# Optimization experiments

Hardware: AMD Instinct MI355X
Metric: run time of the kernel (lower is better)

The kernel has to match this reference:

```python
import jax, jax.numpy as jnp
import numpy as np

H = 1024; W = 1024
SPACE_SIGMA = 16.0; RANGE_SIGMA = 0.25
PAD_XY = 2; PAD_Z = 2
DIM = 5


def setup_inputs() -> dict:
    key = jax.random.key(0)
    k1, k2 = jax.random.split(key)
    features = jax.random.uniform(k1, (H, W, 3), dtype=jnp.float32)
    inp = jax.random.normal(k2, (H, W, 3), dtype=jnp.float32)
    return {"features": features, "inp": inp}


def _grid_dims(features_np):
    # Grid sizes are data-dependent in the original (TF builds them from
    # per-channel min/max); compute them host-side from concrete inputs.
    sh = int(float(H - 1) / SPACE_SIGMA) + 1 + 2 * PAD_XY
    sw = int(float(W - 1) / SPACE_SIGMA) + 1 + 2 * PAD_XY
    depths = []
    for c in range(3):
        ch = features_np[..., c]
        delta = float(ch.max() - ch.min())
        depths.append(int(delta / RANGE_SIGMA) + 1 + 2 * PAD_Z)
    return (sh, sw, depths[0], depths[1], depths[2])


def _both_indices(size, coord):
    left = jnp.clip(coord.astype(jnp.int32), 0, size - 1)
    right = jnp.clip(left + 1, 0, size - 1)
    return left, right


def _convn(data, n_iter=2):
    # Faithful port of the TF convn: separable [1,2,1]/4 pass per axis with
    # the exact same ping-pong buffer / boundary-keep / transpose behavior.
    buffer = jnp.zeros_like(data)
    perm = (1, 2, 3, 4, 0)
    for _ in range(n_iter):
        buffer, data = data, buffer
        for _ in range(DIM):
            newdata = (buffer[:-2] + buffer[2:] + 2.0 * buffer[1:-1]) / 4.0
            data = jnp.concatenate([data[:1], newdata, data[-1:]], axis=0)
            data = jnp.transpose(data, perm)
            buffer = jnp.transpose(buffer, perm)
    return data


def _filter(features, inp, dims):
    sh, sw, dr, dg, db = dims
    hw = H * W
    yy, xx = jnp.meshgrid(jnp.arange(H, dtype=jnp.float32),
                          jnp.arange(W, dtype=jnp.float32), indexing="ij")
    splat_yy = (yy / SPACE_SIGMA + 0.5).astype(jnp.int32) + PAD_XY
    splat_xx = (xx / SPACE_SIGMA + 0.5).astype(jnp.int32) + PAD_XY
    slice_yy = yy / SPACE_SIGMA + PAD_XY
    slice_xx = xx / SPACE_SIGMA + PAD_XY
    y_i, y_i2 = _both_indices(sh, slice_yy)
    x_i, x_i2 = _both_indices(sw, slice_xx)
    y_alpha = (slice_yy - y_i.astype(jnp.float32)).reshape(-1)
    x_alpha = (slice_xx - x_i.astype(jnp.float32)).reshape(-1)

    chans = []
    for c, depth in zip(range(3), (dr, dg, db)):
        v = features[..., c]
        v0 = v - jnp.min(v)
        splat_v = (v0 / RANGE_SIGMA + 0.5).astype(jnp.int32) + PAD_Z
        slice_v = v0 / RANGE_SIGMA + PAD_Z
        li, ri = _both_indices(depth, slice_v)
        alpha = (slice_v - li.astype(jnp.float32)).reshape(-1)
        chans.append((splat_v, li, ri, alpha))
    (splat_rr, r_i, r_i2, r_alpha) = chans[0]
    (splat_gg, g_i, g_i2, g_alpha) = chans[1]
    (splat_bb, b_i, b_i2, b_alpha) = chans[2]

    splat_coords = ((((splat_yy * sw + splat_xx) * dr + splat_rr) * dg
                     + splat_gg) * db + splat_bb).reshape(-1)  # [hw]

    idx_all = jnp.stack([y_i, y_i2, x_i, x_i2, r_i, r_i2,
                         g_i, g_i2, b_i, b_i2]).reshape(10, hw)
    alphas_all = jnp.stack([1.0 - y_alpha, y_alpha, 1.0 - x_alpha, x_alpha,
                            1.0 - r_alpha, r_alpha, 1.0 - g_alpha, g_alpha,
                            1.0 - b_alpha, b_alpha])  # [10, hw]

    # 32 corners of the 5-D hypercube; sel[c, d] picks left/right index per dim.
    corners = np.stack(np.meshgrid(*([np.arange(2)] * DIM), indexing="ij"),
                       axis=-1).reshape(-1, DIM)
    sel = corners + np.arange(DIM) * 2  # [32, 5]

    strides = (sw, dr, dg, db)
    coord = idx_all[sel[:, 0]]  # [32, hw]
    for d in range(1, DIM):
        coord = coord * strides[d - 1] + idx_all[sel[:, d]]
    alpha_prod = alphas_all[sel[:, 0]]  # [32, hw]
    for d in range(1, DIM):
        alpha_prod = alpha_prod * alphas_all[sel[:, d]]

    total = sh * sw * dr * dg * db

    def ch_filter(ch):
        grid = jnp.zeros((total,), jnp.float32).at[splat_coords].add(ch.reshape(-1))
        grid = _convn(grid.reshape(sh, sw, dr, dg, db))
        vals = grid.reshape(-1)[coord]  # [32, hw] multilinear gather
        return jnp.sum(alpha_prod * vals, axis=0).reshape(H, W)

    outT = jax.vmap(ch_filter)(jnp.transpose(inp, (2, 0, 1)))
    return jnp.transpose(outT, (1, 2, 0))


def reference(features, inp):
    dims = _grid_dims(np.asarray(features))
    return _filter(features, inp, dims)
```

## Files before the change

kernel.cpp:

```cpp
#include <hip/hip_runtime.h>

namespace {

constexpr int kH  = 1024;
constexpr int kW  = 1024;
constexpr int kHW = kH * kW;
constexpr int kSH = 68;
constexpr int kSW = 68;
constexpr int kD  = 8;
constexpr int kT3 = kSH * kSW * kD * kD * kD;


__global__ void minmax_kernel(const float* __restrict__ feat, float* __restrict__ part) {
    float mn[3] = {1e30f, 1e30f, 1e30f};
    float mx[3] = {-1e30f, -1e30f, -1e30f};
    int tid = blockIdx.x * blockDim.x + threadIdx.x;
    int stride = gridDim.x * blockDim.x;
    for (int p = tid; p < kHW; p += stride) {
        #pragma unroll
        for (int c = 0; c < 3; ++c) {
            float v = feat[p * 3 + c];
            mn[c] = fminf(mn[c], v);
            mx[c] = fmaxf(mx[c], v);
        }
    }
    #pragma unroll
    for (int off = 32; off > 0; off >>= 1) {
        #pragma unroll
        for (int c = 0; c < 3; ++c) {
            mn[c] = fminf(mn[c], __shfl_down(mn[c], off, 64));
            mx[c] = fmaxf(mx[c], __shfl_down(mx[c], off, 64));
        }
    }
    __shared__ float smn[4][3], smx[4][3];
    int wave = threadIdx.x >> 6;
    if ((threadIdx.x & 63) == 0) {
        #pragma unroll
        for (int c = 0; c < 3; ++c) { smn[wave][c] = mn[c]; smx[wave][c] = mx[c]; }
    }
    __syncthreads();
    if (threadIdx.x == 0) {
        #pragma unroll
        for (int c = 0; c < 3; ++c) {
            part[blockIdx.x * 6 + c]     = fminf(fminf(smn[0][c], smn[1][c]), fminf(smn[2][c], smn[3][c]));
            part[blockIdx.x * 6 + 3 + c] = fmaxf(fmaxf(smx[0][c], smx[1][c]), fmaxf(smx[2][c], smx[3][c]));
        }
    }
}

__global__ void params_kernel(const float* __restrict__ part, float* __restrict__ hdrF) {
    int t = threadIdx.x;
    float mn[3], mx[3];
    #pragma unroll
    for (int c = 0; c < 3; ++c) { mn[c] = part[t * 6 + c]; mx[c] = part[t * 6 + 3 + c]; }
    #pragma unroll
    for (int off = 32; off > 0; off >>= 1) {
        #pragma unroll
        for (int c = 0; c < 3; ++c) {
            mn[c] = fminf(mn[c], __shfl_down(mn[c], off, 64));
            mx[c] = fmaxf(mx[c], __shfl_down(mx[c], off, 64));
        }
    }
    __shared__ float smn[4][3], smx[4][3];
    int wave = t >> 6;
    if ((t & 63) == 0) {
        #pragma unroll
        for (int c = 0; c < 3; ++c) { smn[wave][c] = mn[c]; smx[wave][c] = mx[c]; }
    }
    __syncthreads();
    if (t == 0) {
        int* ip = (int*)(hdrF + 8);
        #pragma unroll
        for (int c = 0; c < 3; ++c) {
            float bmn = fminf(fminf(smn[0][c], smn[1][c]), fminf(smn[2][c], smn[3][c]));
            float bmx = fmaxf(fmaxf(smx[0][c], smx[1][c]), fmaxf(smx[2][c], smx[3][c]));
            float delta = bmx - bmn;
            int depth = (int)((double)delta / 0.25) + 1 + 4;
            if (depth > kD) depth = kD;
            if (depth < 1) depth = 1;
            hdrF[c] = bmn;
            ip[c] = depth;
        }
    }
}

__global__ void splat_kernel(const float* __restrict__ feat,
                             const float* __restrict__ inp,
                             const float* __restrict__ hdrF,
                             float* __restrict__ grid) {
    int ix = blockIdx.x, iy = blockIdx.y;
    int y0 = (iy == 0) ? 0 : 16 * iy - 8;
    int x0 = (ix == 0) ? 0 : 16 * ix - 8;
    int h = (iy == 0 || iy == 64) ? 8 : 16;
    int w = (ix == 0 || ix == 64) ? 8 : 16;

    __shared__ float acc[3 * 512];
    for (int i = threadIdx.x; i < 3 * 512; i += 256) acc[i] = 0.0f;
    __syncthreads();

    int t = threadIdx.x;
    int n = w * h;
    if (t < n) {
        int lx = t & (w - 1);
        int ly = (w == 16) ? (t >> 4) : (t >> 3);
        int y = y0 + ly, x = x0 + lx;
        int p = (y << 10) + x;
        float v0 = feat[p * 3 + 0] - hdrF[0];
        float v1 = feat[p * 3 + 1] - hdrF[1];
        float v2 = feat[p * 3 + 2] - hdrF[2];
        int sr = (int)(v0 * 4.0f + 0.5f) + 2;
        int sg = (int)(v1 * 4.0f + 0.5f) + 2;
        int sb = (int)(v2 * 4.0f + 0.5f) + 2;
        int ci = (sr << 6) + (sg << 3) + sb;
        atomicAdd(&acc[ci],            inp[p * 3 + 0]);
        atomicAdd(&acc[512 + ci],      inp[p * 3 + 1]);
        atomicAdd(&acc[1024 + ci],     inp[p * 3 + 2]);
    }
    __syncthreads();

    long base = ((long)((iy + 2) * kSW + (ix + 2))) << 9;
    for (int i = threadIdx.x; i < 512; i += 256) {
        grid[base + i]            = acc[i];
        grid[kT3 + base + i]      = acc[512 + i];
        grid[2 * kT3 + base + i]  = acc[1024 + i];
    }
}

__global__ __launch_bounds__(192) void blur2_kernel(float* __restrict__ dst,
                                                    const float* __restrict__ src,
                                                    const float* __restrict__ hdrF) {
    int cx = blockIdx.x + 2, cy = blockIdx.y + 2;
    const int* ip = (const int*)(hdrF + 8);
    int dr = ip[0], dg = ip[1], db = ip[2];

    __shared__ float Sv[3 * 512];
    long cbase = ((long)(cy * kSW + cx)) << 9;

    {
        const float4* g4 = (const float4*)src;
        for (int i = threadIdx.x; i < 384; i += 192) {
            int ch = i >> 7, i4 = i & 127;
            float4 q = g4[(long)ch * (kT3 / 4) + (cbase >> 2) + i4];
            int rg = i4 >> 1;
            int b0 = (i4 & 1) * 4;
            Sv[ch * 512 + (b0 + 0) * 64 + rg] = q.x;
            Sv[ch * 512 + (b0 + 1) * 64 + rg] = q.y;
            Sv[ch * 512 + (b0 + 2) * 64 + rg] = q.z;
            Sv[ch * 512 + (b0 + 3) * 64 + rg] = q.w;
        }
    }
    __syncthreads();

    int ch = threadIdx.x >> 6;
    int rg = threadIdx.x & 63;
    int r = rg >> 3, g = rg & 7;

    auto SV = [&](int b, int l) -> float { return Sv[ch * 512 + b * 64 + l]; };
    auto gsp = [&](int ccy, int ccx, int rr, int gg, int bb) -> float {
        if (ccy < 2 || ccy > 66 || ccx < 2 || ccx > 66) return 0.0f;
        return src[(long)ch * kT3 + (((long)(ccy * kSW + ccx)) << 9) + (rr << 6) + (gg << 3) + bb];
    };

    bool gI = (g >= 1) && (g <= dg - 2);
    bool rI = (r >= 1) && (r <= dr - 2);

    float v[8];
    #pragma unroll
    for (int b = 0; b < 8; ++b) v[b] = SV(b, rg);

    int eHi = db - 1;

    auto o1_end = [&](int e) -> float {
        float Vm, Vp;
        if (gI)      { Vm = SV(e, rg - 1); Vp = SV(e, rg + 1); }
        else if (rI) { Vm = SV(e, rg - 8); Vp = SV(e, rg + 8); }
        else         { Vm = gsp(cy, cx - 1, r, g, e); Vp = gsp(cy, cx + 1, r, g, e); }
        return (Vm + Vp + 2.0f * SV(e, rg)) * 0.25f;
    };
    float o1_lo = o1_end(0);
    float o1_hi = o1_end(eHi);

    float o1[8];
    #pragma unroll
    for (int b = 0; b < 8; ++b) {
        float iv = 0.0f;
        if (b >= 1 && b <= 6) iv = ((v[b - 1] + v[b + 1]) + 2.0f * v[b]) * 0.25f;
        o1[b] = (b >= 1 && b <= db - 2) ? iv : (b == 0 ? o1_lo : (b == eHi ? o1_hi : 0.0f));
    }

    auto out1_in = [&](int r2, int g2, int e) -> float {
        int l2 = (r2 << 3) + g2;
        float C = SV(e, l2);
        float Nm, Np;
        if (g2 >= 1 && g2 <= dg - 2)      { Nm = SV(e, l2 - 1); Np = SV(e, l2 + 1); }
        else if (r2 >= 1 && r2 <= dr - 2) { Nm = SV(e, l2 - 8); Np = SV(e, l2 + 8); }
        else { Nm = gsp(cy, cx - 1, r2, g2, e); Np = gsp(cy, cx + 1, r2, g2, e); }
        return (Nm + Np + 2.0f * C) * 0.25f;
    };
    auto out1_x = [&](int cx2, int e) -> float {
        float C = gsp(cy, cx2, r, g, e);
        float Nm, Np;
        if (cx2 >= 1 && cx2 <= kSW - 2) { Nm = gsp(cy, cx2 - 1, r, g, e); Np = gsp(cy, cx2 + 1, r, g, e); }
        else                            { Nm = gsp(cy - 1, cx2, r, g, e); Np = gsp(cy + 1, cx2, r, g, e); }
        return (Nm + Np + 2.0f * C) * 0.25f;
    };

    auto o2_end = [&](int e, float o1e) -> float {
        float Xm, Xp;
        if (gI)      { Xm = out1_in(r, g - 1, e); Xp = out1_in(r, g + 1, e); }
        else if (rI) { Xm = out1_in(r - 1, g, e); Xp = out1_in(r + 1, g, e); }
        else         { Xm = out1_x(cx - 1, e);    Xp = out1_x(cx + 1, e); }
        return (Xm + Xp + 2.0f * o1e) * 0.25f;
    };
    float o2_lo = o2_end(0, o1_lo);
    float o2_hi = o2_end(eHi, o1_hi);

    float o2[8];
    #pragma unroll
    for (int b = 0; b < 8; ++b) {
        float iv = 0.0f;
        if (b >= 1 && b <= 6) iv = ((o1[b - 1] + o1[b + 1]) + 2.0f * o1[b]) * 0.25f;
        o2[b] = (b >= 1 && b <= db - 2) ? iv : (b == 0 ? o2_lo : (b == eHi ? o2_hi : 0.0f));
    }

    __syncthreads();
    #pragma unroll
    for (int b = 0; b < 8; ++b) Sv[ch * 512 + b * 64 + rg] = o2[b];
    __syncthreads();

    {
        float4* d4 = (float4*)dst;
        for (int i = threadIdx.x; i < 384; i += 192) {
            int c2 = i >> 7, i4 = i & 127;
            int l2 = i4 >> 1;
            int b0 = (i4 & 1) * 4;
            float4 q = make_float4(Sv[c2 * 512 + (b0 + 0) * 64 + l2],
                                   Sv[c2 * 512 + (b0 + 1) * 64 + l2],
                                   Sv[c2 * 512 + (b0 + 2) * 64 + l2],
                                   Sv[c2 * 512 + (b0 + 3) * 64 + l2]);
            d4[(long)c2 * (kT3 / 4) + (cbase >> 2) + i4] = q;
        }
    }
}

__global__ __launch_bounds__(256) void slice_kernel(const float* __restrict__ feat,
                                                    const float* __restrict__ hdrF,
                                                    const float* __restrict__ grid,
                                                    float* __restrict__ out) {
    __shared__ float sg[3 * 4 * 512];
    int tx = blockIdx.x, ty = blockIdx.y;

    {
        const float4* g4 = (const float4*)grid;
        float4* s4 = (float4*)sg;
        #pragma unroll
        for (int it = 0; it < 2; ++it) {
            int i = threadIdx.x + it * 256;
            int cell = i >> 7;
            int ci4 = i & 127;
            int cy = ty + 2 + (cell >> 1), cx = tx + 2 + (cell & 1);
            long cbase4 = ((long)(cy * kSW + cx)) << 7;
            #pragma unroll
            for (int ch = 0; ch < 3; ++ch)
                s4[ch * 512 + i] = g4[(long)ch * (kT3 / 4) + cbase4 + ci4];
        }
    }
    __syncthreads();

    const int* ip = (const int*)(hdrF + 8);
    int d3[3] = {ip[0], ip[1], ip[2]};
    int lx = threadIdx.x & 15, ly = threadIdx.x >> 4;
    int y = (ty << 4) + ly, x = (tx << 4) + lx;
    int p = (y << 10) + x;

    float ya = (float)ly * 0.0625f;
    float xa = (float)lx * 0.0625f;

    int li[3], ri[3];
    float al[3];
    #pragma unroll
    for (int c = 0; c < 3; ++c) {
        float v0 = feat[p * 3 + c] - hdrF[c];
        float sv = v0 * 4.0f + 2.0f;
        int l = (int)sv;
        int dm = d3[c] - 1;
        l = l < 0 ? 0 : (l > dm ? dm : l);
        int rr = l + 1 > dm ? dm : l + 1;
        li[c] = l; ri[c] = rr; al[c] = sv - (float)l;
    }

    float spw[4];
    {
        float wy[2] = {1.0f - ya, ya};
        float wx[2] = {1.0f - xa, xa};
        spw[0] = wy[0] * wx[0]; spw[1] = wy[0] * wx[1];
        spw[2] = wy[1] * wx[0]; spw[3] = wy[1] * wx[1];
    }
    int cpi[8]; float cpw[8];
    {
        int rs[2] = {li[0], ri[0]}; float wrr[2] = {1.0f - al[0], al[0]};
        int gs[2] = {li[1], ri[1]}; float wgg[2] = {1.0f - al[1], al[1]};
        int bs[2] = {li[2], ri[2]}; float wbb[2] = {1.0f - al[2], al[2]};
        #pragma unroll
        for (int cr = 0; cr < 2; ++cr)
        #pragma unroll
        for (int cg = 0; cg < 2; ++cg)
        #pragma unroll
        for (int cb = 0; cb < 2; ++cb) {
            int k = (cr * 2 + cg) * 2 + cb;
            cpi[k] = (rs[cr] << 6) + (gs[cg] << 3) + bs[cb];
            cpw[k] = (wrr[cr] * wgg[cg]) * wbb[cb];
        }
    }

    float acc0 = 0.0f, acc1 = 0.0f, acc2 = 0.0f;
    #pragma unroll
    for (int k = 0; k < 4; ++k) {
        #pragma unroll
        for (int j = 0; j < 8; ++j) {
            int si = (k << 9) + cpi[j];
            float w = spw[k] * cpw[j];
            acc0 += w * sg[si];
            acc1 += w * sg[2048 + si];
            acc2 += w * sg[4096 + si];
        }
    }
    out[p * 3 + 0] = acc0;
    out[p * 3 + 1] = acc1;
    out[p * 3 + 2] = acc2;
}

}

extern "C" void kernel_launch(void* const* d_in, const int* in_sizes, int n_in,
                              void* d_out, int out_size, void* d_ws, size_t ws_size,
                              hipStream_t stream) {
    const float* feat = (const float*)d_in[0];
    const float* inp  = (const float*)d_in[1];
    float* out = (float*)d_out;

    float* hdrF  = (float*)d_ws;
    float* part  = (float*)((char*)d_ws + 1024);
    float* gridA = (float*)((char*)d_ws + 8192);
    float* gridB = gridA + 3 * (size_t)kT3;

    minmax_kernel<<<256, 256, 0, stream>>>(feat, part);
    params_kernel<<<1, 256, 0, stream>>>(part, hdrF);

    splat_kernel<<<dim3(65, 65), 256, 0, stream>>>(feat, inp, hdrF, gridA);
    blur2_kernel<<<dim3(65, 65), 192, 0, stream>>>(gridB, gridA, hdrF);
    slice_kernel<<<dim3(64, 64), 256, 0, stream>>>(feat, hdrF, gridB, out);
}
```

Measured before the change: 144.0 us.

## Fuse blur into slice kernel, recomputing blurred cells per tile

Merges the blur and slice kernels: each slice block loads its four neighbouring grid cells, blurs them in shared memory, and slices directly from the blurred values in a transposed layout. This removes one kernel launch and the write and re-read of the intermediate blurred grid, while the blurred values are kept in a b-major layout. In exchange, each cell is blurred up to four times by neighbouring blocks, shared memory use rises to 48KB per block, which limits occupancy, and the per-thread loop runs three blur tasks.

```diff
diff --git a/kernel.cpp b/kernel.cpp
--- a/kernel.cpp
+++ b/kernel.cpp
@@ -126,149 +126,117 @@
     }
 }
 
-__global__ __launch_bounds__(192) void blur2_kernel(float* __restrict__ dst,
-                                                    const float* __restrict__ src,
-                                                    const float* __restrict__ hdrF) {
-    int cx = blockIdx.x + 2, cy = blockIdx.y + 2;
+__global__ __launch_bounds__(256) void blur_slice_kernel(const float* __restrict__ feat,
+                                                         const float* __restrict__ hdrF,
+                                                         const float* __restrict__ src,
+                                                         float* __restrict__ out) {
+    __shared__ float Sv[4 * 1536];
+    __shared__ float Sb[4 * 1536];
+    int tx = blockIdx.x, ty = blockIdx.y;
+
     const int* ip = (const int*)(hdrF + 8);
     int dr = ip[0], dg = ip[1], db = ip[2];
-
-    __shared__ float Sv[3 * 512];
-    long cbase = ((long)(cy * kSW + cx)) << 9;
+    int eHi = db - 1;
 
     {
         const float4* g4 = (const float4*)src;
-        for (int i = threadIdx.x; i < 384; i += 192) {
-            int ch = i >> 7, i4 = i & 127;
-            float4 q = g4[(long)ch * (kT3 / 4) + (cbase >> 2) + i4];
+        for (int i = threadIdx.x; i < 1536; i += 256) {
+            int cell = i / 384;
+            int rem = i - cell * 384;
+            int ch = rem >> 7, i4 = rem & 127;
+            int cy = ty + 2 + (cell >> 1), cx = tx + 2 + (cell & 1);
+            long cb4 = ((long)(cy * kSW + cx)) << 7;
+            float4 q = g4[(long)ch * (kT3 / 4) + cb4 + i4];
             int rg = i4 >> 1;
             int b0 = (i4 & 1) * 4;
-            Sv[ch * 512 + (b0 + 0) * 64 + rg] = q.x;
-            Sv[ch * 512 + (b0 + 1) * 64 + rg] = q.y;
-            Sv[ch * 512 + (b0 + 2) * 64 + rg] = q.z;
-            Sv[ch * 512 + (b0 + 3) * 64 + rg] = q.w;
-        }
-    }
-    __syncthreads();
-
-    int ch = threadIdx.x >> 6;
-    int rg = threadIdx.x & 63;
-    int r = rg >> 3, g = rg & 7;
-
-    auto SV = [&](int b, int l) -> float { return Sv[ch * 512 + b * 64 + l]; };
-    auto gsp = [&](int ccy, int ccx, int rr, int gg, int bb) -> float {
-        if (ccy < 2 || ccy > 66 || ccx < 2 || ccx > 66) return 0.0f;
-        return src[(long)ch * kT3 + (((long)(ccy * kSW + ccx)) << 9) + (rr << 6) + (gg << 3) + bb];
-    };
-
-    bool gI = (g >= 1) && (g <= dg - 2);
-    bool rI = (r >= 1) && (r <= dr - 2);
-
-    float v[8];
-    #pragma unroll
-    for (int b = 0; b < 8; ++b) v[b] = SV(b, rg);
-
-    int eHi = db - 1;
-
-    auto o1_end = [&](int e) -> float {
-        float Vm, Vp;
-        if (gI)      { Vm = SV(e, rg - 1); Vp = SV(e, rg + 1); }
-        else if (rI) { Vm = SV(e, rg - 8); Vp = SV(e, rg + 8); }
-        else         { Vm = gsp(cy, cx - 1, r, g, e); Vp = gsp(cy, cx + 1, r, g, e); }
-        return (Vm + Vp + 2.0f * SV(e, rg)) * 0.25f;
-    };
-    float o1_lo = o1_end(0);
-    float o1_hi = o1_end(eHi);
-
-    float o1[8];
-    #pragma unroll
-    for (int b = 0; b < 8; ++b) {
-        float iv = 0.0f;
-        if (b >= 1 && b <= 6) iv = ((v[b - 1] + v[b + 1]) + 2.0f * v[b]) * 0.25f;
-        o1[b] = (b >= 1 && b <= db - 2) ? iv : (b == 0 ? o1_lo : (b == eHi ? o1_hi : 0.0f));
-    }
-
-    auto out1_in = [&](int r2, int g2, int e) -> float {
-        int l2 = (r2 << 3) + g2;
-        float C = SV(e, l2);
-        float Nm, Np;
-        if (g2 >= 1 && g2 <= dg - 2)      { Nm = SV(e, l2 - 1); Np = SV(e, l2 + 1); }
-        else if (r2 >= 1 && r2 <= dr - 2) { Nm = SV(e, l2 - 8); Np = SV(e, l2 + 8); }
-        else { Nm = gsp(cy, cx - 1, r2, g2, e); Np = gsp(cy, cx + 1, r2, g2, e); }
-        return (Nm + Np + 2.0f * C) * 0.25f;
-    };
-    auto out1_x = [&](int cx2, int e) -> float {
-        float C = gsp(cy, cx2, r, g, e);
-        float Nm, Np;
-        if (cx2 >= 1 && cx2 <= kSW - 2) { Nm = gsp(cy, cx2 - 1, r, g, e); Np = gsp(cy, cx2 + 1, r, g, e); }
-        else                            { Nm = gsp(cy - 1, cx2, r, g, e); Np = gsp(cy + 1, cx2, r, g, e); }
-        return (Nm + Np + 2.0f * C) * 0.25f;
-    };
-
-    auto o2_end = [&](int e, float o1e) -> float {
-        float Xm, Xp;
-        if (gI)      { Xm = out1_in(r, g - 1, e); Xp = out1_in(r, g + 1, e); }
-        else if (rI) { Xm = out1_in(r - 1, g, e); Xp = out1_in(r + 1, g, e); }
-        else         { Xm = out1_x(cx - 1, e);    Xp = out1_x(cx + 1, e); }
-        return (Xm + Xp + 2.0f * o1e) * 0.25f;
-    };
-    float o2_lo = o2_end(0, o1_lo);
-    float o2_hi = o2_end(eHi, o1_hi);
-
-    float o2[8];
-    #pragma unroll
-    for (int b = 0; b < 8; ++b) {
-        float iv = 0.0f;
-        if (b >= 1 && b <= 6) iv = ((o1[b - 1] + o1[b + 1]) + 2.0f * o1[b]) * 0.25f;
-        o2[b] = (b >= 1 && b <= db - 2) ? iv : (b == 0 ? o2_lo : (b == eHi ? o2_hi : 0.0f));
-    }
-
-    __syncthreads();
-    #pragma unroll
-    for (int b = 0; b < 8; ++b) Sv[ch * 512 + b * 64 + rg] = o2[b];
-    __syncthreads();
-
-    {
-        float4* d4 = (float4*)dst;
-        for (int i = threadIdx.x; i < 384; i += 192) {
-            int c2 = i >> 7, i4 = i & 127;
-            int l2 = i4 >> 1;
-            int b0 = (i4 & 1) * 4;
-            float4 q = make_float4(Sv[c2 * 512 + (b0 + 0) * 64 + l2],
-                                   Sv[c2 * 512 + (b0 + 1) * 64 + l2],
-                                   Sv[c2 * 512 + (b0 + 2) * 64 + l2],
-                                   Sv[c2 * 512 + (b0 + 3) * 64 + l2]);
-            d4[(long)c2 * (kT3 / 4) + (cbase >> 2) + i4] = q;
-        }
-    }
-}
-
-__global__ __launch_bounds__(256) void slice_kernel(const float* __restrict__ feat,
-                                                    const float* __restrict__ hdrF,
-                                                    const float* __restrict__ grid,
-                                                    float* __restrict__ out) {
-    __shared__ float sg[3 * 4 * 512];
-    int tx = blockIdx.x, ty = blockIdx.y;
-
-    {
-        const float4* g4 = (const float4*)grid;
-        float4* s4 = (float4*)sg;
-        #pragma unroll
-        for (int it = 0; it < 2; ++it) {
-            int i = threadIdx.x + it * 256;
-            int cell = i >> 7;
-            int ci4 = i & 127;
-            int cy = ty + 2 + (cell >> 1), cx = tx + 2 + (cell & 1);
-            long cbase4 = ((long)(cy * kSW + cx)) << 7;
-            #pragma unroll
-            for (int ch = 0; ch < 3; ++ch)
-                s4[ch * 512 + i] = g4[(long)ch * (kT3 / 4) + cbase4 + ci4];
-        }
-    }
-    __syncthreads();
-
-    const int* ip = (const int*)(hdrF + 8);
-    int d3[3] = {ip[0], ip[1], ip[2]};
+            float* S = Sv + cell * 1536 + ch * 512;
+            S[(b0 + 0) * 64 + rg] = q.x;
+            S[(b0 + 1) * 64 + rg] = q.y;
+            S[(b0 + 2) * 64 + rg] = q.z;
+            S[(b0 + 3) * 64 + rg] = q.w;
+        }
+    }
+    __syncthreads();
+
+    #pragma unroll
+    for (int k = 0; k < 3; ++k) {
+        int task = threadIdx.x + (k << 8);
+        int cell = task / 192;
+        int t2 = task - cell * 192;
+        int ch = t2 >> 6;
+        int rg = t2 & 63;
+        int r = rg >> 3, g = rg & 7;
+        int cy = ty + 2 + (cell >> 1), cx = tx + 2 + (cell & 1);
+
+        float* S = Sv + cell * 1536 + ch * 512;
+        auto SV = [&](int b, int l) -> float { return S[b * 64 + l]; };
+        auto gsp = [&](int ccy, int ccx, int rr, int gg, int bb) -> float {
+            if (ccy < 2 || ccy > 66 || ccx < 2 || ccx > 66) return 0.0f;
+            return src[(long)ch * kT3 + (((long)(ccy * kSW + ccx)) << 9) + (rr << 6) + (gg << 3) + bb];
+        };
+
+        bool gI = (g >= 1) && (g <= dg - 2);
+        bool rI = (r >= 1) && (r <= dr - 2);
+
+        float v[8];
+        #pragma unroll
+        for (int b = 0; b < 8; ++b) v[b] = SV(b, rg);
+
+        auto o1_end = [&](int e) -> float {
+            float Vm, Vp;
+            if (gI)      { Vm = SV(e, rg - 1); Vp = SV(e, rg + 1); }
+            else if (rI) { Vm = SV(e, rg - 8); Vp = SV(e, rg + 8); }
+            else         { Vm = gsp(cy, cx - 1, r, g, e); Vp = gsp(cy, cx + 1, r, g, e); }
+            return (Vm + Vp + 2.0f * SV(e, rg)) * 0.25f;
+        };
+        float o1_lo = o1_end(0);
+        float o1_hi = o1_end(eHi);
+
+        float o1[8];
+        #pragma unroll
+        for (int b = 0; b < 8; ++b) {
+            float iv = 0.0f;
+            if (b >= 1 && b <= 6) iv = ((v[b - 1] + v[b + 1]) + 2.0f * v[b]) * 0.25f;
+            o1[b] = (b >= 1 && b <= db - 2) ? iv : (b == 0 ? o1_lo : (b == eHi ? o1_hi : 0.0f));
+        }
+
+        auto out1_in = [&](int r2, int g2, int e) -> float {
+            int l2 = (r2 << 3) + g2;
+            float C = SV(e, l2);
+            float Nm, Np;
+            if (g2 >= 1 && g2 <= dg - 2)      { Nm = SV(e, l2 - 1); Np = SV(e, l2 + 1); }
+            else if (r2 >= 1 && r2 <= dr - 2) { Nm = SV(e, l2 - 8); Np = SV(e, l2 + 8); }
+            else { Nm = gsp(cy, cx - 1, r2, g2, e); Np = gsp(cy, cx + 1, r2, g2, e); }
+            return (Nm + Np + 2.0f * C) * 0.25f;
+        };
+        auto out1_x = [&](int cx2, int e) -> float {
+            float C = gsp(cy, cx2, r, g, e);
+            float Nm, Np;
+            if (cx2 >= 1 && cx2 <= kSW - 2) { Nm = gsp(cy, cx2 - 1, r, g, e); Np = gsp(cy, cx2 + 1, r, g, e); }
+            else                            { Nm = gsp(cy - 1, cx2, r, g, e); Np = gsp(cy + 1, cx2, r, g, e); }
+            return (Nm + Np + 2.0f * C) * 0.25f;
+        };
+        auto o2_end = [&](int e, float o1e) -> float {
+            float Xm, Xp;
+            if (gI)      { Xm = out1_in(r, g - 1, e); Xp = out1_in(r, g + 1, e); }
+            else if (rI) { Xm = out1_in(r - 1, g, e); Xp = out1_in(r + 1, g, e); }
+            else         { Xm = out1_x(cx - 1, e);    Xp = out1_x(cx + 1, e); }
+            return (Xm + Xp + 2.0f * o1e) * 0.25f;
+        };
+        float o2_lo = o2_end(0, o1_lo);
+        float o2_hi = o2_end(eHi, o1_hi);
+
+        float* B = Sb + cell * 1536 + ch * 512;
+        #pragma unroll
+        for (int b = 0; b < 8; ++b) {
+            float iv = 0.0f;
+            if (b >= 1 && b <= 6) iv = ((o1[b - 1] + o1[b + 1]) + 2.0f * o1[b]) * 0.25f;
+            float o2 = (b >= 1 && b <= db - 2) ? iv : (b == 0 ? o2_lo : (b == eHi ? o2_hi : 0.0f));
+            B[b * 64 + rg] = o2;
+        }
+    }
+    __syncthreads();
+
     int lx = threadIdx.x & 15, ly = threadIdx.x >> 4;
     int y = (ty << 4) + ly, x = (tx << 4) + lx;
     int p = (y << 10) + x;
@@ -278,6 +246,7 @@
 
     int li[3], ri[3];
     float al[3];
+    int d3[3] = {dr, dg, db};
     #pragma unroll
     for (int c = 0; c < 3; ++c) {
         float v0 = feat[p * 3 + c] - hdrF[c];
@@ -308,7 +277,7 @@
         #pragma unroll
         for (int cb = 0; cb < 2; ++cb) {
             int k = (cr * 2 + cg) * 2 + cb;
-            cpi[k] = (rs[cr] << 6) + (gs[cg] << 3) + bs[cb];
+            cpi[k] = (bs[cb] << 6) + (rs[cr] << 3) + gs[cg];
             cpw[k] = (wrr[cr] * wgg[cg]) * wbb[cb];
         }
     }
@@ -316,13 +285,14 @@
     float acc0 = 0.0f, acc1 = 0.0f, acc2 = 0.0f;
     #pragma unroll
     for (int k = 0; k < 4; ++k) {
+        const float* B = Sb + k * 1536;
         #pragma unroll
         for (int j = 0; j < 8; ++j) {
-            int si = (k << 9) + cpi[j];
+            int si = cpi[j];
             float w = spw[k] * cpw[j];
-            acc0 += w * sg[si];
-            acc1 += w * sg[2048 + si];
-            acc2 += w * sg[4096 + si];
+            acc0 += w * B[si];
+            acc1 += w * B[512 + si];
+            acc2 += w * B[1024 + si];
         }
     }
     out[p * 3 + 0] = acc0;
@@ -342,12 +312,10 @@
     float* hdrF  = (float*)d_ws;
     float* part  = (float*)((char*)d_ws + 1024);
     float* gridA = (float*)((char*)d_ws + 8192);
-    float* gridB = gridA + 3 * (size_t)kT3;
 
     minmax_kernel<<<256, 256, 0, stream>>>(feat, part);
     params_kernel<<<1, 256, 0, stream>>>(part, hdrF);
 
     splat_kernel<<<dim3(65, 65), 256, 0, stream>>>(feat, inp, hdrF, gridA);
-    blur2_kernel<<<dim3(65, 65), 192, 0, stream>>>(gridB, gridA, hdrF);
-    slice_kernel<<<dim3(64, 64), 256, 0, stream>>>(feat, hdrF, gridB, out);
-}
+    blur_slice_kernel<<<dim3(64, 64), 256, 0, stream>>>(feat, hdrF, gridA, out);
+}
```

Result: slower. 211.9 us (+47.1%).

## Interleave blurred grid channels as float4 and vectorize splat/minmax loads

Applied to the files above, without the earlier changes.

The blur kernel now writes its output as a compact per-cell float4 array with the three channels interleaved. The slice kernel can then fetch all channels of two adjacent b-corners with two float4 LDS reads and lerp along b, replacing 8 scalar corner gathers per channel. The splat kernel stages features and inputs through shared memory with coalesced float4 loads, and minmax reads float4 vectors. The blur shared buffer is padded to stride 72 to cut bank conflicts, at the cost of extra workspace layout assumptions and a 4th padding lane in the float4 grid.

```diff
diff --git a/kernel.cpp b/kernel.cpp
--- a/kernel.cpp
+++ b/kernel.cpp
@@ -9,20 +9,22 @@
 constexpr int kSW = 68;
 constexpr int kD  = 8;
 constexpr int kT3 = kSH * kSW * kD * kD * kD;
-
+constexpr int kNC = 65;
 
 __global__ void minmax_kernel(const float* __restrict__ feat, float* __restrict__ part) {
+    const float4* f4 = (const float4*)feat;
     float mn[3] = {1e30f, 1e30f, 1e30f};
     float mx[3] = {-1e30f, -1e30f, -1e30f};
     int tid = blockIdx.x * blockDim.x + threadIdx.x;
     int stride = gridDim.x * blockDim.x;
-    for (int p = tid; p < kHW; p += stride) {
-        #pragma unroll
-        for (int c = 0; c < 3; ++c) {
-            float v = feat[p * 3 + c];
-            mn[c] = fminf(mn[c], v);
-            mx[c] = fmaxf(mx[c], v);
-        }
+    for (int c = tid; c < kHW / 4; c += stride) {
+        float4 q0 = f4[c * 3], q1 = f4[c * 3 + 1], q2 = f4[c * 3 + 2];
+        mn[0] = fminf(mn[0], fminf(fminf(q0.x, q0.w), fminf(q1.z, q2.y)));
+        mx[0] = fmaxf(mx[0], fmaxf(fmaxf(q0.x, q0.w), fmaxf(q1.z, q2.y)));
+        mn[1] = fminf(mn[1], fminf(fminf(q0.y, q1.x), fminf(q1.w, q2.z)));
+        mx[1] = fmaxf(mx[1], fmaxf(fmaxf(q0.y, q1.x), fmaxf(q1.w, q2.z)));
+        mn[2] = fminf(mn[2], fminf(fminf(q0.z, q1.y), fminf(q2.x, q2.w)));
+        mx[2] = fmaxf(mx[2], fmaxf(fmaxf(q0.z, q1.y), fmaxf(q2.x, q2.w)));
     }
     #pragma unroll
     for (int off = 32; off > 0; off >>= 1) {
@@ -84,10 +86,10 @@
     }
 }
 
-__global__ void splat_kernel(const float* __restrict__ feat,
-                             const float* __restrict__ inp,
-                             const float* __restrict__ hdrF,
-                             float* __restrict__ grid) {
+__global__ __launch_bounds__(256) void splat_kernel(const float* __restrict__ feat,
+                                                    const float* __restrict__ inp,
+                                                    const float* __restrict__ hdrF,
+                                                    float* __restrict__ grid) {
     int ix = blockIdx.x, iy = blockIdx.y;
     int y0 = (iy == 0) ? 0 : 16 * iy - 8;
     int x0 = (ix == 0) ? 0 : 16 * ix - 8;
@@ -95,7 +97,18 @@
     int w = (ix == 0 || ix == 64) ? 8 : 16;
 
     __shared__ float acc[3 * 512];
+    __shared__ float fS[16 * 48], iS[16 * 48];
     for (int i = threadIdx.x; i < 3 * 512; i += 256) acc[i] = 0.0f;
+
+    int rowVec = (w * 3) >> 2;
+    int nvec = h * rowVec;
+    const float4* f4 = (const float4*)(feat + ((long)y0 * kW + x0) * 3);
+    const float4* i4 = (const float4*)(inp  + ((long)y0 * kW + x0) * 3);
+    for (int t = threadIdx.x; t < nvec; t += 256) {
+        int row = t / rowVec, q = t - row * rowVec;
+        ((float4*)fS)[row * rowVec + q] = f4[row * (kW * 3 / 4) + q];
+        ((float4*)iS)[row * rowVec + q] = i4[row * (kW * 3 / 4) + q];
+    }
     __syncthreads();
 
     int t = threadIdx.x;
@@ -103,18 +116,17 @@
     if (t < n) {
         int lx = t & (w - 1);
         int ly = (w == 16) ? (t >> 4) : (t >> 3);
-        int y = y0 + ly, x = x0 + lx;
-        int p = (y << 10) + x;
-        float v0 = feat[p * 3 + 0] - hdrF[0];
-        float v1 = feat[p * 3 + 1] - hdrF[1];
-        float v2 = feat[p * 3 + 2] - hdrF[2];
+        int o = (ly * w + lx) * 3;
+        float v0 = fS[o + 0] - hdrF[0];
+        float v1 = fS[o + 1] - hdrF[1];
+        float v2 = fS[o + 2] - hdrF[2];
         int sr = (int)(v0 * 4.0f + 0.5f) + 2;
         int sg = (int)(v1 * 4.0f + 0.5f) + 2;
         int sb = (int)(v2 * 4.0f + 0.5f) + 2;
         int ci = (sr << 6) + (sg << 3) + sb;
-        atomicAdd(&acc[ci],            inp[p * 3 + 0]);
-        atomicAdd(&acc[512 + ci],      inp[p * 3 + 1]);
-        atomicAdd(&acc[1024 + ci],     inp[p * 3 + 2]);
+        atomicAdd(&acc[ci],        iS[o + 0]);
+        atomicAdd(&acc[512 + ci],  iS[o + 1]);
+        atomicAdd(&acc[1024 + ci], iS[o + 2]);
     }
     __syncthreads();
 
@@ -126,14 +138,14 @@
     }
 }
 
-__global__ __launch_bounds__(192) void blur2_kernel(float* __restrict__ dst,
+__global__ __launch_bounds__(192) void blur2_kernel(float4* __restrict__ dstB,
                                                     const float* __restrict__ src,
                                                     const float* __restrict__ hdrF) {
     int cx = blockIdx.x + 2, cy = blockIdx.y + 2;
     const int* ip = (const int*)(hdrF + 8);
     int dr = ip[0], dg = ip[1], db = ip[2];
 
-    __shared__ float Sv[3 * 512];
+    __shared__ float Sv[3 * 576];
     long cbase = ((long)(cy * kSW + cx)) << 9;
 
     {
@@ -143,10 +155,11 @@
             float4 q = g4[(long)ch * (kT3 / 4) + (cbase >> 2) + i4];
             int rg = i4 >> 1;
             int b0 = (i4 & 1) * 4;
-            Sv[ch * 512 + (b0 + 0) * 64 + rg] = q.x;
-            Sv[ch * 512 + (b0 + 1) * 64 + rg] = q.y;
-            Sv[ch * 512 + (b0 + 2) * 64 + rg] = q.z;
-            Sv[ch * 512 + (b0 + 3) * 64 + rg] = q.w;
+            float* S = Sv + ch * 576;
+            S[(b0 + 0) * 72 + rg] = q.x;
+            S[(b0 + 1) * 72 + rg] = q.y;
+            S[(b0 + 2) * 72 + rg] = q.z;
+            S[(b0 + 3) * 72 + rg] = q.w;
         }
     }
     __syncthreads();
@@ -155,7 +168,8 @@
     int rg = threadIdx.x & 63;
     int r = rg >> 3, g = rg & 7;
 
-    auto SV = [&](int b, int l) -> float { return Sv[ch * 512 + b * 64 + l]; };
+    float* S = Sv + ch * 576;
+    auto SV = [&](int b, int l) -> float { return S[b * 72 + l]; };
     auto gsp = [&](int ccy, int ccx, int rr, int gg, int bb) -> float {
         if (ccy < 2 || ccy > 66 || ccx < 2 || ccx > 66) return 0.0f;
         return src[(long)ch * kT3 + (((long)(ccy * kSW + ccx)) << 9) + (rr << 6) + (gg << 3) + bb];
@@ -204,7 +218,6 @@
         else                            { Nm = gsp(cy - 1, cx2, r, g, e); Np = gsp(cy + 1, cx2, r, g, e); }
         return (Nm + Np + 2.0f * C) * 0.25f;
     };
-
     auto o2_end = [&](int e, float o1e) -> float {
         float Xm, Xp;
         if (gI)      { Xm = out1_in(r, g - 1, e); Xp = out1_in(r, g + 1, e); }
@@ -225,46 +238,32 @@
 
     __syncthreads();
     #pragma unroll
-    for (int b = 0; b < 8; ++b) Sv[ch * 512 + b * 64 + rg] = o2[b];
-    __syncthreads();
-
-    {
-        float4* d4 = (float4*)dst;
-        for (int i = threadIdx.x; i < 384; i += 192) {
-            int c2 = i >> 7, i4 = i & 127;
-            int l2 = i4 >> 1;
-            int b0 = (i4 & 1) * 4;
-            float4 q = make_float4(Sv[c2 * 512 + (b0 + 0) * 64 + l2],
-                                   Sv[c2 * 512 + (b0 + 1) * 64 + l2],
-                                   Sv[c2 * 512 + (b0 + 2) * 64 + l2],
-                                   Sv[c2 * 512 + (b0 + 3) * 64 + l2]);
-            d4[(long)c2 * (kT3 / 4) + (cbase >> 2) + i4] = q;
-        }
+    for (int b = 0; b < 8; ++b) S[b * 72 + rg] = o2[b];
+    __syncthreads();
+
+    long cellBase = (long)(blockIdx.y * kNC + blockIdx.x) * 512;
+    for (int i = threadIdx.x; i < 512; i += 192) {
+        int b = i & 7, l = i >> 3;
+        dstB[cellBase + i] = make_float4(Sv[b * 72 + l],
+                                         Sv[576 + b * 72 + l],
+                                         Sv[1152 + b * 72 + l],
+                                         0.0f);
     }
 }
 
 __global__ __launch_bounds__(256) void slice_kernel(const float* __restrict__ feat,
                                                     const float* __restrict__ hdrF,
-                                                    const float* __restrict__ grid,
+                                                    const float4* __restrict__ gridB,
                                                     float* __restrict__ out) {
-    __shared__ float sg[3 * 4 * 512];
+    __shared__ float4 Sc[4 * 512 + 1];
     int tx = blockIdx.x, ty = blockIdx.y;
 
-    {
-        const float4* g4 = (const float4*)grid;
-        float4* s4 = (float4*)sg;
-        #pragma unroll
-        for (int it = 0; it < 2; ++it) {
-            int i = threadIdx.x + it * 256;
-            int cell = i >> 7;
-            int ci4 = i & 127;
-            int cy = ty + 2 + (cell >> 1), cx = tx + 2 + (cell & 1);
-            long cbase4 = ((long)(cy * kSW + cx)) << 7;
-            #pragma unroll
-            for (int ch = 0; ch < 3; ++ch)
-                s4[ch * 512 + i] = g4[(long)ch * (kT3 / 4) + cbase4 + ci4];
-        }
-    }
+    for (int i = threadIdx.x; i < 2048; i += 256) {
+        int cell = i >> 9, i4 = i & 511;
+        int cy = ty + (cell >> 1), cx = tx + (cell & 1);
+        Sc[i] = gridB[(long)(cy * kNC + cx) * 512 + i4];
+    }
+    if (threadIdx.x == 0) Sc[2048] = make_float4(0.f, 0.f, 0.f, 0.f);
     __syncthreads();
 
     const int* ip = (const int*)(hdrF + 8);
@@ -296,33 +295,26 @@
         spw[0] = wy[0] * wx[0]; spw[1] = wy[0] * wx[1];
         spw[2] = wy[1] * wx[0]; spw[3] = wy[1] * wx[1];
     }
-    int cpi[8]; float cpw[8];
-    {
-        int rs[2] = {li[0], ri[0]}; float wrr[2] = {1.0f - al[0], al[0]};
-        int gs[2] = {li[1], ri[1]}; float wgg[2] = {1.0f - al[1], al[1]};
-        int bs[2] = {li[2], ri[2]}; float wbb[2] = {1.0f - al[2], al[2]};
+    int rs[2] = {li[0], ri[0]}; float wrr[2] = {1.0f - al[0], al[0]};
+    int gs[2] = {li[1], ri[1]}; float wgg[2] = {1.0f - al[1], al[1]};
+    int bq = li[2];
+    float aeff = (ri[2] > li[2]) ? al[2] : 0.0f;
+
+    float acc0 = 0.0f, acc1 = 0.0f, acc2 = 0.0f;
+    #pragma unroll
+    for (int k = 0; k < 4; ++k) {
+        const float4* C = Sc + (k << 9);
         #pragma unroll
         for (int cr = 0; cr < 2; ++cr)
         #pragma unroll
-        for (int cg = 0; cg < 2; ++cg)
-        #pragma unroll
-        for (int cb = 0; cb < 2; ++cb) {
-            int k = (cr * 2 + cg) * 2 + cb;
-            cpi[k] = (rs[cr] << 6) + (gs[cg] << 3) + bs[cb];
-            cpw[k] = (wrr[cr] * wgg[cg]) * wbb[cb];
-        }
-    }
-
-    float acc0 = 0.0f, acc1 = 0.0f, acc2 = 0.0f;
-    #pragma unroll
-    for (int k = 0; k < 4; ++k) {
-        #pragma unroll
-        for (int j = 0; j < 8; ++j) {
-            int si = (k << 9) + cpi[j];
-            float w = spw[k] * cpw[j];
-            acc0 += w * sg[si];
-            acc1 += w * sg[2048 + si];
-            acc2 += w * sg[4096 + si];
+        for (int cg = 0; cg < 2; ++cg) {
+            int idx = ((rs[cr] << 3) + gs[cg]) * 8 + bq;
+            float4 q0 = C[idx];
+            float4 q1 = C[idx + 1];
+            float w = spw[k] * wrr[cr] * wgg[cg];
+            acc0 += w * (q0.x + aeff * (q1.x - q0.x));
+            acc1 += w * (q0.y + aeff * (q1.y - q0.y));
+            acc2 += w * (q0.z + aeff * (q1.z - q0.z));
         }
     }
     out[p * 3 + 0] = acc0;
@@ -339,10 +331,10 @@
     const float* inp  = (const float*)d_in[1];
     float* out = (float*)d_out;
 
-    float* hdrF  = (float*)d_ws;
-    float* part  = (float*)((char*)d_ws + 1024);
-    float* gridA = (float*)((char*)d_ws + 8192);
-    float* gridB = gridA + 3 * (size_t)kT3;
+    float*  hdrF  = (float*)d_ws;
+    float*  part  = (float*)((char*)d_ws + 1024);
+    float*  gridA = (float*)((char*)d_ws + 8192);
+    float4* gridB = (float4*)((char*)d_ws + 8192 + 3 * (size_t)kT3 * sizeof(float));
 
     minmax_kernel<<<256, 256, 0, stream>>>(feat, part);
     params_kernel<<<1, 256, 0, stream>>>(part, hdrF);
```

Measured after the change: 150.7 us. 1.05x slower.
